# Optimization experiments

Measured on AMD Instinct MI355X. Metric: run time of the kernel, lower is better.

## Reference

```python
import jax, jax.numpy as jnp
import numpy as np

B, D, C, L, H = 4096, 768, 512, 32, 256
E = C * L  # total flattened extension embeddings

def _l2norm(x, eps=1e-12):
    n = jnp.sqrt(jnp.sum(x * x, axis=-1, keepdims=True))
    return x / jnp.maximum(n, eps)

def setup_inputs() -> dict:
    key = jax.random.key(0)
    ks = jax.random.split(key, 8)
    text_feat = jax.random.normal(ks[0], (B, D), dtype=jnp.float32)
    img_feat = jax.random.normal(ks[1], (B, D), dtype=jnp.float32)
    ext_embs = _l2norm(jax.random.normal(ks[2], (E, D), dtype=jnp.float32))
    concept_names = _l2norm(jax.random.normal(ks[3], (C, D), dtype=jnp.float32))
    # each concept has exactly L extension embeddings; sorted segment ids
    segment_ids = jnp.repeat(jnp.arange(C, dtype=jnp.int32), L)
    W1 = jax.random.normal(ks[4], (C + D, H), dtype=jnp.float32) * (1.0 / np.sqrt(C + D))
    b1 = jnp.zeros((H,), dtype=jnp.float32)
    W2 = jax.random.normal(ks[5], (H, C), dtype=jnp.float32) * (1.0 / np.sqrt(H))
    b2 = jnp.zeros((C,), dtype=jnp.float32)
    alpha = jnp.float32(0.5)
    temperature = jnp.float32(0.07)
    return {"text_feat": text_feat, "img_feat": img_feat, "ext_embs": ext_embs,
            "segment_ids": segment_ids, "concept_names": concept_names,
            "W1": W1, "b1": b1, "W2": W2, "b2": b2,
            "alpha": alpha, "temperature": temperature}

def reference(text_feat, img_feat, ext_embs, segment_ids, concept_names,
              W1, b1, W2, b2, alpha, temperature):
    # query = normalize(text + img)
    q = _l2norm(text_feat + img_feat)                      # [B, D]
    # ragged per-concept max similarity: one big GEMM + segmented max
    sim = jnp.einsum('bd,ed->be', q, ext_embs)            # [B, E]
    prior = jax.ops.segment_max(sim.T, segment_ids,
                                num_segments=C,
                                indices_are_sorted=True).T  # [B, C]
    # small MLP -> temperature softmax -> weighted concept sum
    h = jax.nn.relu(jnp.concatenate([prior, q], axis=-1) @ W1 + b1)  # [B, H]
    logits = h @ W2 + b2                                   # [B, C]
    weights = jax.nn.softmax(logits / temperature, axis=-1)
    dyn_prompt = weights @ concept_names                   # [B, D]
    combined = text_feat + alpha * dyn_prompt
    return _l2norm(combined)
```

## Files before the change

### kernel.cpp

```cpp
#include <hip/hip_runtime.h>
#include <hip/hip_bf16.h>

typedef unsigned short bfu;
typedef __attribute__((ext_vector_type(4))) float f32x4;
typedef __attribute__((ext_vector_type(8))) short bf16x8;
typedef __attribute__((ext_vector_type(4))) int i32x4;
typedef __attribute__((ext_vector_type(8))) int i32x8;

__device__ __forceinline__ unsigned short f2bf(float f) {
    unsigned int u = __float_as_uint(f);
    u += 0x7FFFu + ((u >> 16) & 1u);
    return (unsigned short)(u >> 16);
}

__device__ __forceinline__ unsigned pack_fp8x4(float a, float b, float c, float d) {
    int u = __builtin_amdgcn_cvt_pk_fp8_f32(a, b, 0, false);
    u = __builtin_amdgcn_cvt_pk_fp8_f32(c, d, u, true);
    return (unsigned)u;
}

__device__ __forceinline__ void gload_lds16(const void* g, void* l) {
    __builtin_amdgcn_global_load_lds(
        (const __attribute__((address_space(1))) unsigned int*)g,
        (__attribute__((address_space(3))) unsigned int*)l, 16, 0, 0);
}

__device__ __forceinline__ float block_sum256(float v, float* sm) {
    #pragma unroll
    for (int off = 32; off; off >>= 1) v += __shfl_xor(v, off);
    int w = threadIdx.x >> 6;
    if ((threadIdx.x & 63) == 0) sm[w] = v;
    __syncthreads();
    float r = sm[0] + sm[1] + sm[2] + sm[3];
    __syncthreads();
    return r;
}

__device__ __forceinline__ float block_max256(float v, float* sm) {
    #pragma unroll
    for (int off = 32; off; off >>= 1) v = fmaxf(v, __shfl_xor(v, off));
    int w = threadIdx.x >> 6;
    if ((threadIdx.x & 63) == 0) sm[w] = v;
    __syncthreads();
    float r = fmaxf(fmaxf(sm[0], sm[1]), fmaxf(sm[2], sm[3]));
    __syncthreads();
    return r;
}

__global__ __launch_bounds__(256) void prep_kernel(const float* __restrict__ text,
                                                   const float* __restrict__ img,
                                                   bfu* __restrict__ X,
                                                   unsigned* __restrict__ Q8,
                                                   const float* __restrict__ ext,
                                                   unsigned* __restrict__ E8,
                                                   const float* __restrict__ W1, bfu* __restrict__ W1t,
                                                   const float* __restrict__ W2, bfu* __restrict__ W2t,
                                                   const float* __restrict__ cn, bfu* __restrict__ cnt) {
    __shared__ float sm[4];
    int b = blockIdx.x, t = threadIdx.x;
    if (b < 4096) {
        int row = b;
        float4 v = {0.f, 0.f, 0.f, 0.f};
        if (t < 192) {
            float4 a = ((const float4*)(text + (size_t)row * 768))[t];
            float4 c = ((const float4*)(img + (size_t)row * 768))[t];
            v.x = a.x + c.x; v.y = a.y + c.y; v.z = a.z + c.z; v.w = a.w + c.w;
        }
        float ss = v.x * v.x + v.y * v.y + v.z * v.z + v.w * v.w;
        float tot = block_sum256(ss, sm);
        float inv = 1.0f / fmaxf(sqrtf(tot), 1e-12f);
        if (t < 192) {
            ushort4 o = make_ushort4(f2bf(v.x * inv), f2bf(v.y * inv), f2bf(v.z * inv), f2bf(v.w * inv));
            ((ushort4*)(X + (size_t)row * 1280 + 512))[t] = o;
            float s16 = inv * 16.0f;
            Q8[(size_t)row * 192 + t] = pack_fp8x4(v.x * s16, v.y * s16, v.z * s16, v.w * s16);
        }
    } else if (b < 16384) {
        int i = (b - 4096) * 256 + t;
        float4 v = ((const float4*)ext)[i];
        E8[i] = pack_fp8x4(v.x * 16.0f, v.y * 16.0f, v.z * 16.0f, v.w * 16.0f);
    } else if (b < 17664) {
        int idx = (b - 16384) * 256 + t;
        int c = idx / 1280, r = idx - c * 1280;
        W1t[idx] = f2bf(W1[(size_t)r * 256 + c]);
    } else if (b < 18176) {
        int idx = (b - 17664) * 256 + t;
        int c = idx / 256, r = idx - c * 256;
        W2t[idx] = f2bf(W2[(size_t)r * 512 + c]);
    } else {
        int idx = (b - 18176) * 256 + t;
        int c = idx / 512, r = idx - c * 512;
        cnt[idx] = f2bf(cn[(size_t)r * 768 + c]);
    }
}

__device__ __forceinline__ i32x8 ld_frag8(const char* s, int row, int lq) {
    const int r7 = row & 7;
    i32x4 lo = *(const i32x4*)(s + row * 128 + ((((lq << 1))     ^ r7) << 4));
    i32x4 hi = *(const i32x4*)(s + row * 128 + ((((lq << 1) | 1) ^ r7) << 4));
    i32x8 v;
    v[0] = lo[0]; v[1] = lo[1]; v[2] = lo[2]; v[3] = lo[3];
    v[4] = hi[0]; v[5] = hi[1]; v[6] = hi[2]; v[7] = hi[3];
    return v;
}

__global__ __launch_bounds__(512) void sim_segmax_kernel(const unsigned char* __restrict__ Q8,
                                                         const unsigned char* __restrict__ E8,
                                                         bfu* __restrict__ X) {
    __shared__ __align__(16) char sA[2][128 * 128];
    __shared__ __align__(16) char sB[2][128 * 128];
    const int bm = blockIdx.x & 31;
    const int bn = blockIdx.x >> 5;
    const int m0 = bm << 7, n0 = bn << 7;
    const int t = threadIdx.x, lane = t & 63, wv = t >> 6;
    const int wm = (wv >> 2) << 6;
    const int wn = (wv & 3) << 5;
    const int lr = lane & 15, lq = lane >> 4;

    f32x4 zero = {0.f, 0.f, 0.f, 0.f};
    f32x4 acc[4][2];
    #pragma unroll
    for (int i = 0; i < 4; ++i)
        #pragma unroll
        for (int j = 0; j < 2; ++j) acc[i][j] = zero;

    auto stage = [&](int slot, int k0) {
        char* bufA = sA[slot];
        char* bufB = sB[slot];
        #pragma unroll
        for (int i = 0; i < 2; ++i) {
            int idx = (i << 9) + t;
            int row = idx >> 3, c = idx & 7, cs = c ^ (row & 7);
            gload_lds16(Q8 + (size_t)(m0 + row) * 768 + k0 + (cs << 4),
                        bufA + (((i << 9) + (wv << 6)) << 4));
        }
        #pragma unroll
        for (int i = 0; i < 2; ++i) {
            int idx = (i << 9) + t;
            int row = idx >> 3, c = idx & 7, cs = c ^ (row & 7);
            gload_lds16(E8 + (size_t)(n0 + row) * 768 + k0 + (cs << 4),
                        bufB + (((i << 9) + (wv << 6)) << 4));
        }
    };

    stage(0, 0);
    stage(1, 128);
    __builtin_amdgcn_sched_barrier(0);
    asm volatile("s_waitcnt vmcnt(4)" ::: "memory");
    __builtin_amdgcn_sched_barrier(0);
    __builtin_amdgcn_s_barrier();
    __builtin_amdgcn_sched_barrier(0);

    #pragma unroll
    for (int kk = 0; kk < 6; ++kk) {
        if (kk >= 1 && kk <= 4) stage((kk + 1) & 1, (kk + 1) << 7);
        const char* bufA = sA[kk & 1];
        const char* bufB = sB[kk & 1];
        i32x8 af[4], bf[2];
        #pragma unroll
        for (int f = 0; f < 4; ++f)
            af[f] = ld_frag8(bufA, wm + f * 16 + lr, lq);
        #pragma unroll
        for (int j = 0; j < 2; ++j)
            bf[j] = ld_frag8(bufB, wn + j * 16 + lr, lq);
        #pragma unroll
        for (int i = 0; i < 4; ++i)
            #pragma unroll
            for (int j = 0; j < 2; ++j)
                acc[i][j] = __builtin_amdgcn_mfma_scale_f32_16x16x128_f8f6f4(
                    af[i], bf[j], acc[i][j], 0, 0, 0, 0x7F7F7F7F, 0, 0x7F7F7F7F);
        if (kk < 5) {
            __builtin_amdgcn_sched_barrier(0);
            asm volatile("s_waitcnt vmcnt(0)" ::: "memory");
            asm volatile("s_waitcnt lgkmcnt(0)" ::: "memory");
            __builtin_amdgcn_sched_barrier(0);
            __builtin_amdgcn_s_barrier();
            __builtin_amdgcn_sched_barrier(0);
        }
    }

    const float sc = 0.00390625f;
    const int g = (n0 + wn) >> 5;
    #pragma unroll
    for (int i = 0; i < 4; ++i) {
        #pragma unroll
        for (int r = 0; r < 4; ++r) {
            float v = fmaxf(acc[i][0][r], acc[i][1][r]);
            #pragma unroll
            for (int off = 8; off; off >>= 1)
                v = fmaxf(v, __shfl_xor(v, off));
            if (lr == 0) {
                int row = m0 + wm + i * 16 + lq * 4 + r;
                X[(size_t)row * 1280 + g] = f2bf(v * sc);
            }
        }
    }
}

template <int BM>
__device__ __forceinline__ void gemm_mainloop(const bfu* A, const bfu* B, int K,
                                              int lda, int ldb, int m0, int n0,
                                              short* sA, short* sB, f32x4 acc[BM / 32][4]) {
    const int t = threadIdx.x, lane = t & 63, wv = t >> 6;
    const int wm = (wv >> 1) * (BM / 2), wn = (wv & 1) << 6;
    const int lr = lane & 15, lq = lane >> 4;

    i32x4 ra[BM / 32], rb[4];
    auto ldg = [&](int k0) {
        #pragma unroll
        for (int i = 0; i < BM / 32; ++i) {
            int idx = i * 256 + t;
            int row = idx >> 3, cg = idx & 7;
            ra[i] = *(const i32x4*)(A + (size_t)(m0 + row) * lda + k0 + (cg << 3));
        }
        #pragma unroll
        for (int i = 0; i < 4; ++i) {
            int idx = i * 256 + t;
            int row = idx >> 3, cg = idx & 7;
            rb[i] = *(const i32x4*)(B + (size_t)(n0 + row) * ldb + k0 + (cg << 3));
        }
    };
    auto st_lds = [&]() {
        #pragma unroll
        for (int i = 0; i < BM / 32; ++i) {
            int idx = i * 256 + t;
            int row = idx >> 3, cg = idx & 7, cs = cg ^ (row & 7);
            *(i32x4*)(sA + row * 64 + cs * 8) = ra[i];
        }
        #pragma unroll
        for (int i = 0; i < 4; ++i) {
            int idx = i * 256 + t;
            int row = idx >> 3, cg = idx & 7, cs = cg ^ (row & 7);
            *(i32x4*)(sB + row * 64 + cs * 8) = rb[i];
        }
    };

    const int NIT = K >> 6;
    ldg(0);
    for (int kk = 0; kk < NIT; ++kk) {
        if (kk) __syncthreads();
        st_lds();
        __syncthreads();
        if (kk + 1 < NIT) ldg((kk + 1) * 64);
        #pragma unroll
        for (int ks = 0; ks < 2; ++ks) {
            bf16x8 af[BM / 32], bfr[4];
            #pragma unroll
            for (int f = 0; f < BM / 32; ++f) {
                int mrow = wm + f * 16 + lr;
                int c = ks * 4 + lq;
                af[f] = *(const bf16x8*)(sA + mrow * 64 + ((c ^ (mrow & 7)) << 3));
            }
            #pragma unroll
            for (int f = 0; f < 4; ++f) {
                int nrow = wn + f * 16 + lr;
                int c = ks * 4 + lq;
                bfr[f] = *(const bf16x8*)(sB + nrow * 64 + ((c ^ (nrow & 7)) << 3));
            }
            #pragma unroll
            for (int i = 0; i < BM / 32; ++i)
                #pragma unroll
                for (int j = 0; j < 4; ++j)
                    acc[i][j] = __builtin_amdgcn_mfma_f32_16x16x32_bf16(af[i], bfr[j], acc[i][j], 0, 0, 0);
        }
    }
}

template <int EPI, int BM>
__global__ __launch_bounds__(256) void gemm_kernel(const bfu* __restrict__ A,
                                                   const bfu* __restrict__ B,
                                                   const float* __restrict__ bias,
                                                   void* __restrict__ out,
                                                   int K, int lda, int ldb, int N, int ntN) {
    __shared__ __align__(16) short sA[BM * 64];
    __shared__ __align__(16) short sB[128 * 64];
    int bm = blockIdx.x / ntN, bn = blockIdx.x - bm * ntN;
    int m0 = bm * BM, n0 = bn * 128;
    f32x4 zero = {0.f, 0.f, 0.f, 0.f};
    f32x4 acc[BM / 32][4];
    #pragma unroll
    for (int i = 0; i < BM / 32; ++i)
        #pragma unroll
        for (int j = 0; j < 4; ++j) acc[i][j] = zero;

    gemm_mainloop<BM>(A, B, K, lda, ldb, m0, n0, sA, sB, acc);

    const int t = threadIdx.x, lane = t & 63, wv = t >> 6;
    const int wm = (wv >> 1) * (BM / 2), wn = (wv & 1) << 6;
    const int lr = lane & 15, lq = lane >> 4;
    #pragma unroll
    for (int j = 0; j < 4; ++j) {
        int col = n0 + wn + j * 16 + lr;
        float bv = (EPI >= 1) ? bias[col] : 0.0f;
        #pragma unroll
        for (int i = 0; i < BM / 32; ++i) {
            #pragma unroll
            for (int r = 0; r < 4; ++r) {
                int row = m0 + wm + i * 16 + lq * 4 + r;
                float v = acc[i][j][r] + bv;
                if (EPI == 1) {
                    v = fmaxf(v, 0.0f);
                    ((bfu*)out)[(size_t)row * N + col] = f2bf(v);
                } else {
                    ((float*)out)[(size_t)row * N + col] = v;
                }
            }
        }
    }
}

__global__ __launch_bounds__(256) void softmax_kernel(const float* __restrict__ logits,
                                                      const float* __restrict__ temp,
                                                      bfu* __restrict__ wout) {
    __shared__ float sm[4];
    int row = blockIdx.x, t = threadIdx.x;
    float invT = 1.0f / temp[0];
    float l0 = logits[(size_t)row * 512 + t];
    float l1 = logits[(size_t)row * 512 + 256 + t];
    float m = block_max256(fmaxf(l0, l1), sm);
    float e0 = __expf((l0 - m) * invT);
    float e1 = __expf((l1 - m) * invT);
    float s = block_sum256(e0 + e1, sm);
    float inv = 1.0f / s;
    wout[(size_t)row * 512 + t]       = f2bf(e0 * inv);
    wout[(size_t)row * 512 + 256 + t] = f2bf(e1 * inv);
}

__global__ __launch_bounds__(256) void final_kernel(const float* __restrict__ text,
                                                    const float* __restrict__ dyn,
                                                    const float* __restrict__ alpha,
                                                    float* __restrict__ out) {
    __shared__ float sm[4];
    int row = blockIdx.x, t = threadIdx.x;
    float a = alpha[0];
    float v[3]; float ss = 0.f;
    #pragma unroll
    for (int i = 0; i < 3; ++i) {
        size_t o = (size_t)row * 768 + t + 256 * i;
        v[i] = text[o] + a * dyn[o];
        ss += v[i] * v[i];
    }
    float tot = block_sum256(ss, sm);
    float inv = 1.0f / fmaxf(sqrtf(tot), 1e-12f);
    #pragma unroll
    for (int i = 0; i < 3; ++i)
        out[(size_t)row * 768 + t + 256 * i] = v[i] * inv;
}

extern "C" void kernel_launch(void* const* d_in, const int* in_sizes, int n_in,
                              void* d_out, int out_size, void* d_ws, size_t ws_size,
                              hipStream_t stream) {
    const float* text  = (const float*)d_in[0];
    const float* img   = (const float*)d_in[1];
    const float* ext   = (const float*)d_in[2];
    const float* cn    = (const float*)d_in[4];
    const float* W1    = (const float*)d_in[5];
    const float* b1    = (const float*)d_in[6];
    const float* W2    = (const float*)d_in[7];
    const float* b2    = (const float*)d_in[8];
    const float* alpha = (const float*)d_in[9];
    const float* temp  = (const float*)d_in[10];
    float* out = (float*)d_out;

    char* p = (char*)d_ws;
    auto carve = [&](size_t bytes) -> char* {
        char* r = p; p += (bytes + 255) & ~(size_t)255; return r;
    };
    unsigned char* E8 = (unsigned char*)carve((size_t)16384 * 768);
    unsigned char* Q8 = (unsigned char*)carve((size_t)4096 * 768);
    bfu*   X      = (bfu*)carve((size_t)4096 * 1280 * 2);
    bfu*   W1t    = (bfu*)carve((size_t)256 * 1280 * 2);
    bfu*   W2t    = (bfu*)carve((size_t)512 * 256 * 2);
    bfu*   cnt    = (bfu*)carve((size_t)768 * 512 * 2);
    bfu*   Hm     = (bfu*)carve((size_t)4096 * 256 * 2);
    float* logits = (float*)carve((size_t)4096 * 512 * 4);
    bfu*   wts    = (bfu*)carve((size_t)4096 * 512 * 2);
    float* dyn    = (float*)carve((size_t)4096 * 768 * 4);

    prep_kernel<<<19712, 256, 0, stream>>>(text, img, X, (unsigned*)Q8,
                                           ext, (unsigned*)E8, W1, W1t, W2, W2t, cn, cnt);
    sim_segmax_kernel<<<4096, 512, 0, stream>>>(Q8, E8, X);
    gemm_kernel<1, 32><<<128 * 2, 256, 0, stream>>>(X, W1t, b1, (void*)Hm, 1280, 1280, 1280, 256, 2);
    gemm_kernel<2, 64><<<64 * 4, 256, 0, stream>>>(Hm, W2t, b2, (void*)logits, 256, 256, 256, 512, 4);
    softmax_kernel<<<4096, 256, 0, stream>>>(logits, temp, wts);
    gemm_kernel<0, 64><<<64 * 6, 256, 0, stream>>>(wts, cnt, nullptr, (void*)dyn, 512, 512, 512, 768, 6);
    final_kernel<<<4096, 256, 0, stream>>>(text, dyn, alpha, out);
}
```

Measured before the change: 290.2 us.

## Widen sim GEMM K-stage to 256 and enlarge W1 GEMM tile

The FP8 similarity GEMM now stages 256-wide K slices per double-buffered step, so it runs 3 iterations instead of 6 and needs half as many block barriers and waitcnt stalls. The load mapping and fragment addressing are rewritten to match the 256-byte LDS rows. This doubles LDS use to 128KB per block, which may cut occupancy and leave less load/compute overlap. Separately, the first MLP GEMM switches to a 64-row tile with half the blocks.

```diff
diff --git a/kernel.cpp b/kernel.cpp
--- a/kernel.cpp
+++ b/kernel.cpp
@@ -94,10 +94,11 @@
     }
 }
 
-__device__ __forceinline__ i32x8 ld_frag8(const char* s, int row, int lq) {
+__device__ __forceinline__ i32x8 ld_frag256(const char* s, int row, int lq, int ks) {
     const int r7 = row & 7;
-    i32x4 lo = *(const i32x4*)(s + row * 128 + ((((lq << 1))     ^ r7) << 4));
-    i32x4 hi = *(const i32x4*)(s + row * 128 + ((((lq << 1) | 1) ^ r7) << 4));
+    const int base = row * 256 + (ks << 7);
+    i32x4 lo = *(const i32x4*)(s + base + ((((lq << 1))     ^ r7) << 4));
+    i32x4 hi = *(const i32x4*)(s + base + ((((lq << 1) | 1) ^ r7) << 4));
     i32x8 v;
     v[0] = lo[0]; v[1] = lo[1]; v[2] = lo[2]; v[3] = lo[3];
     v[4] = hi[0]; v[5] = hi[1]; v[6] = hi[2]; v[7] = hi[3];
@@ -107,8 +108,8 @@
 __global__ __launch_bounds__(512) void sim_segmax_kernel(const unsigned char* __restrict__ Q8,
                                                          const unsigned char* __restrict__ E8,
                                                          bfu* __restrict__ X) {
-    __shared__ __align__(16) char sA[2][128 * 128];
-    __shared__ __align__(16) char sB[2][128 * 128];
+    __shared__ __align__(16) char sA[2][128 * 256];
+    __shared__ __align__(16) char sB[2][128 * 256];
     const int bm = blockIdx.x & 31;
     const int bn = blockIdx.x >> 5;
     const int m0 = bm << 7, n0 = bn << 7;
@@ -125,51 +126,54 @@
         for (int j = 0; j < 2; ++j) acc[i][j] = zero;
 
     auto stage = [&](int slot, int k0) {
-        char* bufA = sA[slot];
-        char* bufB = sB[slot];
-        #pragma unroll
-        for (int i = 0; i < 2; ++i) {
-            int idx = (i << 9) + t;
-            int row = idx >> 3, c = idx & 7, cs = c ^ (row & 7);
-            gload_lds16(Q8 + (size_t)(m0 + row) * 768 + k0 + (cs << 4),
-                        bufA + (((i << 9) + (wv << 6)) << 4));
-        }
-        #pragma unroll
-        for (int i = 0; i < 2; ++i) {
-            int idx = (i << 9) + t;
-            int row = idx >> 3, c = idx & 7, cs = c ^ (row & 7);
-            gload_lds16(E8 + (size_t)(n0 + row) * 768 + k0 + (cs << 4),
-                        bufB + (((i << 9) + (wv << 6)) << 4));
+        int row = t >> 4, c = t & 15;
+        int cs = c ^ (row & 7);
+        const unsigned char* gA = Q8 + (size_t)(m0 + row) * 768 + k0 + (cs << 4);
+        const unsigned char* gB = E8 + (size_t)(n0 + row) * 768 + k0 + (cs << 4);
+        char* lA = sA[slot] + (wv << 10);
+        char* lB = sB[slot] + (wv << 10);
+        #pragma unroll
+        for (int i = 0; i < 4; ++i) {
+            gload_lds16(gA, lA);
+            gA += 32 * 768; lA += 512 * 16;
+        }
+        #pragma unroll
+        for (int i = 0; i < 4; ++i) {
+            gload_lds16(gB, lB);
+            gB += 32 * 768; lB += 512 * 16;
         }
     };
 
     stage(0, 0);
-    stage(1, 128);
+    stage(1, 256);
     __builtin_amdgcn_sched_barrier(0);
-    asm volatile("s_waitcnt vmcnt(4)" ::: "memory");
+    asm volatile("s_waitcnt vmcnt(8)" ::: "memory");
     __builtin_amdgcn_sched_barrier(0);
     __builtin_amdgcn_s_barrier();
     __builtin_amdgcn_sched_barrier(0);
 
     #pragma unroll
-    for (int kk = 0; kk < 6; ++kk) {
-        if (kk >= 1 && kk <= 4) stage((kk + 1) & 1, (kk + 1) << 7);
+    for (int kk = 0; kk < 3; ++kk) {
+        if (kk == 1) stage(0, 512);
         const char* bufA = sA[kk & 1];
         const char* bufB = sB[kk & 1];
-        i32x8 af[4], bf[2];
-        #pragma unroll
-        for (int f = 0; f < 4; ++f)
-            af[f] = ld_frag8(bufA, wm + f * 16 + lr, lq);
-        #pragma unroll
-        for (int j = 0; j < 2; ++j)
-            bf[j] = ld_frag8(bufB, wn + j * 16 + lr, lq);
-        #pragma unroll
-        for (int i = 0; i < 4; ++i)
+        #pragma unroll
+        for (int ks = 0; ks < 2; ++ks) {
+            i32x8 af[4], bf[2];
+            #pragma unroll
+            for (int f = 0; f < 4; ++f)
+                af[f] = ld_frag256(bufA, wm + f * 16 + lr, lq, ks);
             #pragma unroll
             for (int j = 0; j < 2; ++j)
-                acc[i][j] = __builtin_amdgcn_mfma_scale_f32_16x16x128_f8f6f4(
-                    af[i], bf[j], acc[i][j], 0, 0, 0, 0x7F7F7F7F, 0, 0x7F7F7F7F);
-        if (kk < 5) {
+                bf[j] = ld_frag256(bufB, wn + j * 16 + lr, lq, ks);
+            #pragma unroll
+            for (int i = 0; i < 4; ++i)
+                #pragma unroll
+                for (int j = 0; j < 2; ++j)
+                    acc[i][j] = __builtin_amdgcn_mfma_scale_f32_16x16x128_f8f6f4(
+                        af[i], bf[j], acc[i][j], 0, 0, 0, 0x7F7F7F7F, 0, 0x7F7F7F7F);
+        }
+        if (kk < 2) {
             __builtin_amdgcn_sched_barrier(0);
             asm volatile("s_waitcnt vmcnt(0)" ::: "memory");
             asm volatile("s_waitcnt lgkmcnt(0)" ::: "memory");
@@ -380,7 +384,7 @@
     prep_kernel<<<19712, 256, 0, stream>>>(text, img, X, (unsigned*)Q8,
                                            ext, (unsigned*)E8, W1, W1t, W2, W2t, cn, cnt);
     sim_segmax_kernel<<<4096, 512, 0, stream>>>(Q8, E8, X);
-    gemm_kernel<1, 32><<<128 * 2, 256, 0, stream>>>(X, W1t, b1, (void*)Hm, 1280, 1280, 1280, 256, 2);
+    gemm_kernel<1, 64><<<64 * 2, 256, 0, stream>>>(X, W1t, b1, (void*)Hm, 1280, 1280, 1280, 256, 2);
     gemm_kernel<2, 64><<<64 * 4, 256, 0, stream>>>(Hm, W2t, b2, (void*)logits, 256, 256, 256, 512, 4);
     softmax_kernel<<<4096, 256, 0, stream>>>(logits, temp, wts);
     gemm_kernel<0, 64><<<64 * 6, 256, 0, stream>>>(wts, cnt, nullptr, (void*)dyn, 512, 512, 512, 768, 6);
```

New measurement: 275.3 us. -5.1%, faster.
